# Kernel optimization log

Hardware: AMD Instinct MI355X
Metric: run time of the kernel (lower is better)

Reference implementation:

```python
import jax, jax.numpy as jnp
from jax import lax
import numpy as np

HID = 64      # hidden_size
IND = 25      # input_dim = 10 static + 15 dynamic features
HW = 25       # spatial size fixed by fc1 = Linear(12*12*hidden, ...)


def setup_inputs() -> dict:
    key = jax.random.key(0)
    ks = jax.random.split(key, 8)
    def rn(k, shape, s=0.05):
        return jax.random.normal(k, shape, dtype=jnp.float32) * s
    B, T = 64, 24
    return {
        "x": jax.random.normal(ks[0], (B, T, IND, HW, HW), dtype=jnp.float32),
        "ln_g": jnp.ones((IND,), jnp.float32),
        "ln_b": jnp.zeros((IND,), jnp.float32),
        "w_lstm1": rn(ks[1], (4 * HID, IND + HID, 3, 3)),
        "b_lstm1": jnp.zeros((4 * HID,), jnp.float32),
        "w_lstm2": rn(ks[2], (4 * HID, IND + HID, 3, 3)),
        "b_lstm2": jnp.zeros((4 * HID,), jnp.float32),
        "w_conv": rn(ks[3], (HID, 2 * HID, 3, 3)),
        "b_conv": jnp.zeros((HID,), jnp.float32),
        "w_fc1": rn(ks[4], (HID, 12 * 12 * HID)),
        "b_fc1": jnp.zeros((HID,), jnp.float32),
        "w_fc2": rn(ks[5], (HID // 2, HID)),
        "b_fc2": jnp.zeros((HID // 2,), jnp.float32),
        "w_fc3": rn(ks[6], (2, HID // 2)),
        "b_fc3": jnp.zeros((2,), jnp.float32),
    }


def _convlstm(x, w, b, dil):
    # x: (B, T, C, H, W); one ConvLSTM layer, zero-initialized states.
    # Gate order i, f, o, g (standard ndrplz ConvLSTM); same-padding 3x3 conv
    # with rhs dilation `dil` (padding = dil keeps HxW).
    B, _, _, H, W = x.shape
    h0 = jnp.zeros((B, HID, H, W), x.dtype)

    def step(carry, xt):
        h, c = carry
        z = lax.conv_general_dilated(
            jnp.concatenate([xt, h], axis=1), w, (1, 1),
            [(dil, dil), (dil, dil)], rhs_dilation=(dil, dil))
        z = z + b[None, :, None, None]
        i, f, o, g = jnp.split(z, 4, axis=1)
        c = jax.nn.sigmoid(f) * c + jax.nn.sigmoid(i) * jnp.tanh(g)
        h = jax.nn.sigmoid(o) * jnp.tanh(c)
        return (h, c), None

    (h, _), _ = lax.scan(step, (h0, h0), jnp.moveaxis(x, 1, 0))
    return h  # final hidden state (B, HID, H, W)


def reference(x, ln_g, ln_b, w_lstm1, b_lstm1, w_lstm2, b_lstm2,
              w_conv, b_conv, w_fc1, b_fc1, w_fc2, b_fc2, w_fc3, b_fc3):
    # LayerNorm over the channel dim (torch permutes C to last, LN, permutes back)
    mu = jnp.mean(x, axis=2, keepdims=True)
    var = jnp.var(x, axis=2, keepdims=True)
    xn = (x - mu) * lax.rsqrt(var + 1e-5)
    xn = xn * ln_g[None, None, :, None, None] + ln_b[None, None, :, None, None]

    h1 = _convlstm(xn, w_lstm1, b_lstm1, 1)   # dilation 1 branch
    h2 = _convlstm(xn, w_lstm2, b_lstm2, 2)   # dilation 2 branch
    h = jnp.concatenate([h1, h2], axis=1)     # (B, 2*HID, 25, 25)

    h = lax.conv_general_dilated(h, w_conv, (1, 1), [(1, 1), (1, 1)])
    h = jax.nn.relu(h + b_conv[None, :, None, None])
    # max_pool2d(2): floor(25/2)=12 -> VALID window 2 stride 2
    h = lax.reduce_window(h, -jnp.inf, lax.max, (1, 1, 2, 2), (1, 1, 2, 2), 'VALID')
    h = h.reshape(h.shape[0], -1)             # (B, 12*12*HID), channel-major like torch
    h = jax.nn.relu(h @ w_fc1.T + b_fc1)      # dropout is identity at inference
    h = jax.nn.relu(h @ w_fc2.T + b_fc2)
    h = h @ w_fc3.T + b_fc3
    return jax.nn.log_softmax(h, axis=1)
```

## Files before the change

kernel.cpp:

```cpp
#include <hip/hip_runtime.h>
#include <hip/hip_bf16.h>
#include <math.h>

#define B_    64
#define T_    24
#define IND_  25
#define HID_  64
#define NPIX  625

#define WP0   27
#define WP1   29
#define XSTR  32
#define HSTR  72
#define XROWS0 800
#define XROWS1 912
#define HROWS0 800
#define HROWS1 912
#define XB0   (XROWS0*XSTR)
#define XB1   (XROWS1*XSTR)
#define HB0   (HROWS0*HSTR)
#define HB1   (HROWS1*HSTR)
#define XB0T  (B_*XB0)
#define XB1T  (B_*XB1)
#define HB0T  (B_*HB0)
#define HB1T  (B_*HB1)
#define HPART (HB0T+HB1T)

#define NRG   9
#define RST0  144
#define RST1  212
#define CH0   (RST0*9)
#define CH1   (RST1*9)
#define XCH0  (RST0*4)
#define XCH1  (RST1*4)

#define HCROWS 832
#define HCB    (HCROWS*128)
#define HCTOT  (B_*HCB)

#define WFRAG_PER_BR (9*3*4*4*512)
#define WFRAG_TOT    (2*WFRAG_PER_BR)

typedef __bf16 bf16x8 __attribute__((ext_vector_type(8)));
typedef float  f32x4  __attribute__((ext_vector_type(4)));
typedef unsigned short ushort_t;
typedef unsigned int   uint_t;

typedef const __attribute__((address_space(1))) void as1_cvoid;
typedef __attribute__((address_space(3))) void as3_void;

__device__ __forceinline__ float sigmoidf_(float x) { return 1.f / (1.f + __expf(-x)); }
__device__ __forceinline__ float tanh_fast(float x) { return 2.f / (1.f + __expf(-2.f * x)) - 1.f; }
__device__ __forceinline__ ushort_t f2bf(float f) {
    unsigned int u = __float_as_uint(f);
    u += 0x7FFFu + ((u >> 16) & 1u);
    return (ushort_t)(u >> 16);
}

__global__ __launch_bounds__(256) void fill_zero_kernel(uint_t* __restrict__ p, int n) {
    int i = blockIdx.x * 256 + threadIdx.x;
    if (i < n) p[i] = 0u;
}

__global__ __launch_bounds__(256) void repack_w_kernel(
    const float* __restrict__ w1, const float* __restrict__ w2, ushort_t* __restrict__ Wfrag)
{
    int id = blockIdx.x * 256 + threadIdx.x;
    if (id >= WFRAG_TOT) return;
    int e    = id & 7;
    int lane = (id >> 3) & 63;
    int mf   = (id >> 9) & 3;
    int wm   = (id >> 11) & 3;
    int rest = id >> 13;
    int kk   = rest % 3;
    int tap  = (rest / 3) % 9;
    int br   = rest / 27;
    int l16 = lane & 15, kh = lane >> 4;
    int gate = mf;
    int oc   = wm * 16 + l16;
    int k    = kh * 8 + e;
    int c;
    if (kk == 0)      c = (k < IND_) ? k : -1;
    else if (kk == 1) c = IND_ + k;
    else              c = IND_ + 32 + k;
    const float* w = br ? w2 : w1;
    float v = (c >= 0) ? w[((size_t)(gate * 64 + oc) * 89 + c) * 9 + tap] : 0.f;
    Wfrag[id] = f2bf(v);
}

__global__ __launch_bounds__(256) void repack_wc_kernel(
    const float* __restrict__ wc, ushort_t* __restrict__ Wc)
{
    int id = blockIdx.x * 256 + threadIdx.x;
    if (id >= 9 * 64 * 128) return;
    int k   = id % 128;
    int oc  = (id / 128) % 64;
    int tap = id / (128 * 64);
    Wc[id] = f2bf(wc[((size_t)(oc * 128) + k) * 9 + tap]);
}

__global__ __launch_bounds__(256) void ln_t_kernel(
    const float* __restrict__ x, const float* __restrict__ gamma, const float* __restrict__ beta,
    ushort_t* __restrict__ xb0, ushort_t* __restrict__ xb1, int t)
{
    int p = blockIdx.x * 256 + threadIdx.x;
    if (p >= B_ * NPIX) return;
    int b = p / NPIX, hw = p % NPIX;
    int y = hw / 25, xx = hw % 25;
    const float* xp = x + ((size_t)(b * T_ + t) * IND_) * NPIX + hw;
    float v[IND_];
    float s = 0.f;
#pragma unroll
    for (int c = 0; c < IND_; ++c) { v[c] = xp[c * NPIX]; s += v[c]; }
    float mu = s * (1.f / IND_);
    float ss = 0.f;
#pragma unroll
    for (int c = 0; c < IND_; ++c) { float d = v[c] - mu; ss += d * d; }
    float rstd = rsqrtf(ss * (1.f / IND_) + 1e-5f);
    ushort_t* o0 = xb0 + (size_t)b * XB0 + (size_t)((y + 1) * WP0 + (xx + 1)) * XSTR;
    ushort_t* o1 = xb1 + (size_t)b * XB1 + (size_t)((y + 2) * WP1 + (xx + 2)) * XSTR;
#pragma unroll
    for (int c = 0; c < IND_; ++c) {
        ushort_t hv = f2bf((v[c] - mu) * rstd * gamma[c] + beta[c]);
        o0[c] = hv;
        o1[c] = hv;
    }
}

__global__ __launch_bounds__(512, 4) void convlstm_mfma_kernel(
    const float* __restrict__ x, const float* __restrict__ ln_g, const float* __restrict__ ln_b,
    ushort_t* __restrict__ xb0g, ushort_t* __restrict__ xb1g,
    const ushort_t* __restrict__ h0c, const ushort_t* __restrict__ h1c,
    ushort_t* __restrict__ h0n, ushort_t* __restrict__ h1n,
    const ushort_t* __restrict__ Wfrag,
    const float* __restrict__ bias1, const float* __restrict__ bias2,
    float* __restrict__ cst, int t)
{
    const int rg = blockIdx.x;
    const int b  = blockIdx.y;
    const int br = blockIdx.z;
    const int d  = 1 + br;
    const int Wp = 25 + 2 * d;
    const int par = t & 1, nxt = par ^ 1;
    const ushort_t* __restrict__ hc = (br ? h1c + (size_t)b * HB1 : h0c + (size_t)b * HB0);
    ushort_t* __restrict__ hn       = (br ? h1n + (size_t)b * HB1 : h0n + (size_t)b * HB0);
    const ushort_t* __restrict__ xbcur =
        br ? (xb1g + (size_t)par * XB1T + (size_t)b * XB1)
           : (xb0g + (size_t)par * XB0T + (size_t)b * XB0);
    const float* __restrict__ bias = br ? bias2 : bias1;
    const ushort_t* __restrict__ WFb = Wfrag + (size_t)br * WFRAG_PER_BR;
    f32x4* __restrict__ cb4 = (f32x4*)cst + (size_t)(br * B_ + b) * 16 * NPIX;

    __shared__ ushort_t tile[RST1 * HSTR];
    __shared__ ushort_t xtile[RST1 * XSTR];

    const int tid = threadIdx.x;
    const int u0  = rg * 3 * Wp;
    const int CH  = br ? CH1 : CH0;
    const int XCH = br ? XCH1 : XCH0;
    const int wave_u = tid & 448;

    {
        const char* gsrc = (const char*)(hc + (size_t)u0 * HSTR);
#pragma unroll
        for (int j = 0; j < 4; ++j) {
            const int i = j * 512 + tid;
            if (i < CH) {
                __builtin_amdgcn_global_load_lds(
                    (as1_cvoid*)(gsrc + (size_t)i * 16),
                    (as3_void*)((char*)tile + (size_t)(j * 512 + wave_u) * 16),
                    16, 0, 0);
            }
        }
    }
    {
        const char* gsrc = (const char*)(xbcur + (size_t)u0 * XSTR);
#pragma unroll
        for (int j = 0; j < 2; ++j) {
            const int i = j * 512 + tid;
            if (i < XCH) {
                __builtin_amdgcn_global_load_lds(
                    (as1_cvoid*)(gsrc + (size_t)i * 16),
                    (as3_void*)((char*)xtile + (size_t)(j * 512 + wave_u) * 16),
                    16, 0, 0);
            }
        }
    }
    if (t + 1 < T_ && tid < 35) {
        const int linbid = (br * B_ + b) * NRG + rg;
        const int p = linbid * 35 + tid;
        if (p < B_ * NPIX) {
            const int bb = p / NPIX, hw = p - bb * NPIX;
            const int y = hw / 25, xx = hw - y * 25;
            const float* xp = x + ((size_t)(bb * T_ + t + 1) * IND_) * NPIX + hw;
            float v[IND_];
            float s = 0.f;
#pragma unroll
            for (int c = 0; c < IND_; ++c) { v[c] = xp[c * NPIX]; s += v[c]; }
            const float mu = s * (1.f / IND_);
            float ss = 0.f;
#pragma unroll
            for (int c = 0; c < IND_; ++c) { float dd = v[c] - mu; ss += dd * dd; }
            const float rstd = rsqrtf(ss * (1.f / IND_) + 1e-5f);
            ushort_t us[IND_];
#pragma unroll
            for (int c = 0; c < IND_; ++c) us[c] = f2bf((v[c] - mu) * rstd * ln_g[c] + ln_b[c]);
            uint4 q0, q1, q2;
            q0.x = us[0] | ((uint_t)us[1] << 16);   q0.y = us[2] | ((uint_t)us[3] << 16);
            q0.z = us[4] | ((uint_t)us[5] << 16);   q0.w = us[6] | ((uint_t)us[7] << 16);
            q1.x = us[8] | ((uint_t)us[9] << 16);   q1.y = us[10] | ((uint_t)us[11] << 16);
            q1.z = us[12] | ((uint_t)us[13] << 16); q1.w = us[14] | ((uint_t)us[15] << 16);
            q2.x = us[16] | ((uint_t)us[17] << 16); q2.y = us[18] | ((uint_t)us[19] << 16);
            q2.z = us[20] | ((uint_t)us[21] << 16); q2.w = us[22] | ((uint_t)us[23] << 16);
            ushort_t* o0 = xb0g + (size_t)nxt * XB0T + (size_t)bb * XB0
                           + (size_t)((y + 1) * WP0 + (xx + 1)) * XSTR;
            ushort_t* o1 = xb1g + (size_t)nxt * XB1T + (size_t)bb * XB1
                           + (size_t)((y + 2) * WP1 + (xx + 2)) * XSTR;
            *(uint4*)o0 = q0; *(uint4*)(o0 + 8) = q1; *(uint4*)(o0 + 16) = q2; o0[24] = us[24];
            *(uint4*)o1 = q0; *(uint4*)(o1 + 8) = q1; *(uint4*)(o1 + 16) = q2; o1[24] = us[24];
        }
    }
    __syncthreads();

    const int w    = tid >> 6, lane = tid & 63;
    const int wm   = w & 3, wn = w >> 2;
    const int l16  = lane & 15, kh = lane >> 4;
    const int koff = kh * 8;

    f32x4 acc[4][3];
#pragma unroll
    for (int i = 0; i < 4; ++i)
#pragma unroll
        for (int j = 0; j < 3; ++j) acc[i][j] = (f32x4){0.f, 0.f, 0.f, 0.f};

    int baserel[3];
#pragma unroll
    for (int nf = 0; nf < 3; ++nf) {
        int n = wn * 48 + nf * 16 + l16;
        baserel[nf] = (n >> 5) * Wp + (n & 31);
    }

    const ushort_t* __restrict__ WTb = WFb + wm * 2048 + lane * 8;
    bf16x8 af[2][4];
#pragma unroll
    for (int mf = 0; mf < 4; ++mf)
        af[0][mf] = *(const bf16x8*)(WTb + mf * 512);

#pragma unroll
    for (int u = 0; u < 27; ++u) {
        if (u + 1 < 27) {
#pragma unroll
            for (int mf = 0; mf < 4; ++mf)
                af[(u + 1) & 1][mf] =
                    *(const bf16x8*)(WTb + (size_t)(u + 1) * 8192 + mf * 512);
        }
        const int tap = u / 3, kk = u - 3 * (u / 3);
        const int ky = tap / 3, kx = tap - 3 * ky;
        const int toff = (ky * Wp + kx) * d;
        bf16x8 bfr[3];
        if (kk == 0) {
#pragma unroll
            for (int nf = 0; nf < 3; ++nf)
                bfr[nf] = *(const bf16x8*)(xtile + (size_t)(baserel[nf] + toff) * XSTR + koff);
        } else {
#pragma unroll
            for (int nf = 0; nf < 3; ++nf)
                bfr[nf] = *(const bf16x8*)(tile + (baserel[nf] + toff) * HSTR
                                           + (kk - 1) * 32 + koff);
        }
#pragma unroll
        for (int mf = 0; mf < 4; ++mf)
#pragma unroll
            for (int nf = 0; nf < 3; ++nf)
                acc[mf][nf] = __builtin_amdgcn_mfma_f32_16x16x32_bf16(
                    af[u & 1][mf], bfr[nf], acc[mf][nf], 0, 0, 0);
    }

    const int oc0 = wm * 16 + kh * 4;
    const int ocq = wm * 4 + kh;
    float bi4[4], bf4[4], bo4[4], bg4[4];
#pragma unroll
    for (int r = 0; r < 4; ++r) {
        bi4[r] = bias[oc0 + r];
        bf4[r] = bias[64 + oc0 + r];
        bo4[r] = bias[128 + oc0 + r];
        bg4[r] = bias[192 + oc0 + r];
    }
#pragma unroll
    for (int nf = 0; nf < 3; ++nf) {
        const int n = wn * 48 + nf * 16 + l16;
        const int xx = n & 31;
        if (xx >= 25) continue;
        const int y = rg * 3 + (n >> 5);
        if (y >= 25) continue;
        const int pix = y * 25 + xx;
        f32x4* cp = cb4 + (size_t)ocq * NPIX + pix;
        f32x4 cv;
        if (t != 0) cv = *cp;
        else        cv = (f32x4){0.f, 0.f, 0.f, 0.f};
        ushort_t hs[4];
#pragma unroll
        for (int r = 0; r < 4; ++r) {
            const float zi = acc[0][nf][r] + bi4[r];
            const float zf = acc[1][nf][r] + bf4[r];
            const float zo = acc[2][nf][r] + bo4[r];
            const float zg = acc[3][nf][r] + bg4[r];
            const float cn = sigmoidf_(zf) * cv[r] + sigmoidf_(zi) * tanh_fast(zg);
            cv[r] = cn;
            hs[r] = f2bf(sigmoidf_(zo) * tanh_fast(cn));
        }
        *cp = cv;
        uint2 hv;
        hv.x = (uint_t)hs[0] | ((uint_t)hs[1] << 16);
        hv.y = (uint_t)hs[2] | ((uint_t)hs[3] << 16);
        *(uint2*)(hn + (size_t)((y + d) * Wp + (xx + d)) * HSTR + oc0) = hv;
    }
}

__global__ __launch_bounds__(256) void combine_h_kernel(
    const ushort_t* __restrict__ h0, const ushort_t* __restrict__ h1, ushort_t* __restrict__ Hc)
{
    int id = blockIdx.x * 256 + threadIdx.x;
    if (id >= B_ * NPIX * 128) return;
    int k   = id % 128;
    int pix = (id / 128) % NPIX;
    int b   = id / (128 * NPIX);
    int y = pix / 25, xx = pix % 25;
    ushort_t v;
    if (k < 64) v = h0[(size_t)b * HB0 + (size_t)((y + 1) * WP0 + (xx + 1)) * HSTR + k];
    else        v = h1[(size_t)b * HB1 + (size_t)((y + 2) * WP1 + (xx + 2)) * HSTR + (k - 64)];
    Hc[(size_t)b * HCB + (size_t)((y + 1) * 27 + (xx + 1)) * 128 + k] = v;
}

__global__ __launch_bounds__(512) void conv_mfma_kernel(
    const ushort_t* __restrict__ Hc, const ushort_t* __restrict__ Wc,
    const float* __restrict__ bc, float* __restrict__ conv_out)
{
    const int rg = blockIdx.x;
    const int b  = blockIdx.y;
    const ushort_t* __restrict__ Hb = Hc + (size_t)b * HCB;

    const int tid  = threadIdx.x;
    const int w    = tid >> 6, lane = tid & 63;
    const int wm   = w & 1, wn = w >> 1;
    const int l16  = lane & 15, kh = lane >> 4;
    const int koff = kh * 8;

    f32x4 acc[2][2];
#pragma unroll
    for (int i = 0; i < 2; ++i)
#pragma unroll
        for (int j = 0; j < 2; ++j) acc[i][j] = (f32x4){0.f, 0.f, 0.f, 0.f};

    int baserow[2];
#pragma unroll
    for (int nf = 0; nf < 2; ++nf) {
        int n = wn * 32 + nf * 16 + l16;
        baserow[nf] = (rg * 4 + (n >> 5)) * 27 + (n & 31);
    }
    const ushort_t* __restrict__ Wm = Wc + (size_t)(wm * 32 + l16) * 128 + koff;

    for (int tap = 0; tap < 9; ++tap) {
        const int ky = tap / 3, kx = tap - 3 * ky;
        const int toff = ky * 27 + kx;
        const ushort_t* __restrict__ Wt = Wm + (size_t)tap * (64 * 128);
        const ushort_t* Urow[2];
#pragma unroll
        for (int nf = 0; nf < 2; ++nf)
            Urow[nf] = Hb + (size_t)(baserow[nf] + toff) * 128 + koff;
#pragma unroll
        for (int kk = 0; kk < 4; ++kk) {
            bf16x8 af[2], bfr[2];
#pragma unroll
            for (int mf = 0; mf < 2; ++mf)
                af[mf] = *(const bf16x8*)(Wt + mf * 16 * 128 + kk * 32);
#pragma unroll
            for (int nf = 0; nf < 2; ++nf)
                bfr[nf] = *(const bf16x8*)(Urow[nf] + kk * 32);
#pragma unroll
            for (int mf = 0; mf < 2; ++mf)
#pragma unroll
                for (int nf = 0; nf < 2; ++nf)
                    acc[mf][nf] = __builtin_amdgcn_mfma_f32_16x16x32_bf16(
                        af[mf], bfr[nf], acc[mf][nf], 0, 0, 0);
        }
    }

#pragma unroll
    for (int mf = 0; mf < 2; ++mf) {
#pragma unroll
        for (int nf = 0; nf < 2; ++nf) {
            const int n = wn * 32 + nf * 16 + l16;
            const int xx = n & 31;
            if (xx >= 25) continue;
            const int y = rg * 4 + wn;
            if (y >= 25) continue;
#pragma unroll
            for (int r = 0; r < 4; ++r) {
                const int oc = wm * 32 + mf * 16 + kh * 4 + r;
                const float v = fmaxf(acc[mf][nf][r] + bc[oc], 0.f);
                conv_out[((size_t)(b * 64 + oc)) * NPIX + y * 25 + xx] = v;
            }
        }
    }
}

__global__ __launch_bounds__(256) void pool_kernel(
    const float* __restrict__ conv_out, float* __restrict__ pool)
{
    int id = blockIdx.x * 256 + threadIdx.x;
    if (id >= B_ * 64 * 144) return;
    int px = id % 12;
    int py = (id / 12) % 12;
    int oc = (id / 144) % 64;
    int b  = id / (144 * 64);
    const float* p = conv_out + ((size_t)(b * 64 + oc)) * NPIX;
    const int cy = 2 * py, cx = 2 * px;
    float mx = fmaxf(fmaxf(p[cy * 25 + cx], p[cy * 25 + cx + 1]),
                     fmaxf(p[(cy + 1) * 25 + cx], p[(cy + 1) * 25 + cx + 1]));
    pool[(size_t)b * 9216 + oc * 144 + py * 12 + px] = mx;
}

__global__ __launch_bounds__(256) void fc1_kernel(
    const float* __restrict__ pool, const float* __restrict__ w1, const float* __restrict__ b1,
    float* __restrict__ f1)
{
    const int task = blockIdx.x * 4 + (threadIdx.x >> 6);
    const int lane = threadIdx.x & 63;
    const int b = task >> 6, oc = task & 63;
    const float* pr = pool + (size_t)b * 9216;
    const float* wr = w1 + (size_t)oc * 9216;
    float acc = 0.f;
#pragma unroll 4
    for (int it = 0; it < 36; ++it) {
        const int k = it * 256 + lane * 4;
        const float4 p = *(const float4*)(pr + k);
        const float4 ww = *(const float4*)(wr + k);
        acc += p.x * ww.x + p.y * ww.y + p.z * ww.z + p.w * ww.w;
    }
#pragma unroll
    for (int off = 32; off > 0; off >>= 1) acc += __shfl_down(acc, off);
    if (lane == 0) f1[b * 64 + oc] = fmaxf(acc + b1[oc], 0.f);
}

__global__ __launch_bounds__(64) void head2_kernel(
    const float* __restrict__ f1,
    const float* __restrict__ w2, const float* __restrict__ b2,
    const float* __restrict__ w3, const float* __restrict__ b3,
    float* __restrict__ out)
{
    const int b = blockIdx.x;
    __shared__ float f1l[64];
    __shared__ float f2[32];
    const int tid = threadIdx.x;
    f1l[tid] = f1[b * 64 + tid];
    __syncthreads();
    if (tid < 32) {
        float acc = b2[tid];
        const float* wr = w2 + (size_t)tid * 64;
#pragma unroll
        for (int k = 0; k < 64; ++k) acc += f1l[k] * wr[k];
        f2[tid] = fmaxf(acc, 0.f);
    }
    __syncthreads();
    if (tid == 0) {
        float y0 = b3[0], y1 = b3[1];
#pragma unroll
        for (int k = 0; k < 32; ++k) { y0 += f2[k] * w3[k]; y1 += f2[k] * w3[32 + k]; }
        const float m = fmaxf(y0, y1);
        const float lse = m + logf(expf(y0 - m) + expf(y1 - m));
        out[b * 2 + 0] = y0 - lse;
        out[b * 2 + 1] = y1 - lse;
    }
}

extern "C" void kernel_launch(void* const* d_in, const int* in_sizes, int n_in,
                              void* d_out, int out_size, void* d_ws, size_t ws_size,
                              hipStream_t stream) {
    const float* x    = (const float*)d_in[0];
    const float* ln_g = (const float*)d_in[1];
    const float* ln_b = (const float*)d_in[2];
    const float* w_l1 = (const float*)d_in[3];
    const float* b_l1 = (const float*)d_in[4];
    const float* w_l2 = (const float*)d_in[5];
    const float* b_l2 = (const float*)d_in[6];
    const float* w_c  = (const float*)d_in[7];
    const float* b_c  = (const float*)d_in[8];
    const float* w_f1 = (const float*)d_in[9];
    const float* b_f1 = (const float*)d_in[10];
    const float* w_f2 = (const float*)d_in[11];
    const float* b_f2 = (const float*)d_in[12];
    const float* w_f3 = (const float*)d_in[13];
    const float* b_f3 = (const float*)d_in[14];

    ushort_t* wsu = (ushort_t*)d_ws;
    uint_t*   wsi = (uint_t*)d_ws;

    ushort_t* xb0 = wsu;
    ushort_t* xb1 = xb0 + 2 * (size_t)XB0T;
    ushort_t* h0A = xb1 + 2 * (size_t)XB1T;
    ushort_t* h1A = h0A + HB0T;
    ushort_t* h0B = h1A + HB1T;
    ushort_t* h1B = h0B + HB0T;
    float*    cst = (float*)(h1B + HB1T);
    float*    conv_out = cst;
    float*    pool = cst + 2560000;
    ushort_t* Wfrag = (ushort_t*)cst + 10240000;
    ushort_t* Wc    = Wfrag + WFRAG_TOT;
    float*    f1    = (float*)(Wc + 73728);
    ushort_t* Hc    = h0B;

    const size_t zt = 2 * (size_t)XB0T + 2 * (size_t)XB1T + 2 * (size_t)HPART;
    fill_zero_kernel<<<((int)(zt / 2) + 255) / 256, 256, 0, stream>>>(wsi, (int)(zt / 2));
    repack_w_kernel<<<(WFRAG_TOT + 255) / 256, 256, 0, stream>>>(w_l1, w_l2, Wfrag);
    repack_wc_kernel<<<(9 * 64 * 128 + 255) / 256, 256, 0, stream>>>(w_c, Wc);

    ln_t_kernel<<<(B_ * NPIX + 255) / 256, 256, 0, stream>>>(x, ln_g, ln_b, xb0, xb1, 0);

    ushort_t* H0[2] = {h0A, h0B};
    ushort_t* H1[2] = {h1A, h1B};
    for (int t = 0; t < T_; ++t) {
        const int cur = t & 1, nxt = cur ^ 1;
        convlstm_mfma_kernel<<<dim3(NRG, B_, 2), 512, 0, stream>>>(
            x, ln_g, ln_b, xb0, xb1,
            H0[cur], H1[cur], H0[nxt], H1[nxt], Wfrag, b_l1, b_l2, cst, t);
    }
    fill_zero_kernel<<<(HCTOT / 2 + 255) / 256, 256, 0, stream>>>((uint_t*)Hc, HCTOT / 2);
    combine_h_kernel<<<(B_ * NPIX * 128 + 255) / 256, 256, 0, stream>>>(h0A, h1A, Hc);
    conv_mfma_kernel<<<dim3(7, B_), 512, 0, stream>>>(Hc, Wc, b_c, conv_out);
    pool_kernel<<<(B_ * 64 * 144 + 255) / 256, 256, 0, stream>>>(conv_out, pool);
    fc1_kernel<<<1024, 256, 0, stream>>>(pool, w_f1, b_f1, f1);
    head2_kernel<<<B_, 64, 0, stream>>>(f1, w_f2, b_f2, w_f3, b_f3, (float*)d_out);
}
```

Before: 1.925 ms.

## Unify padded x buffer, read x directly from global, store cell state in fp16

Replaces the two per-branch padded bf16 input buffers with one buffer padded by 2, so each pixel's normalized input is written once. The convlstm kernel no longer stages the x tile in LDS and reads x fragments straight from global or L2 instead, which cuts LDS usage and the async load. The cell state is stored in fp16 rather than fp32, halving its read and write traffic each timestep. The trade-offs are uncoalesced global reads inside the MFMA loop and reduced precision in the recurrent cell state.

```diff
diff --git a/kernel.cpp b/kernel.cpp
--- a/kernel.cpp
+++ b/kernel.cpp
@@ -10,29 +10,25 @@
 
 #define WP0   27
 #define WP1   29
-#define XSTR  32
 #define HSTR  72
-#define XROWS0 800
-#define XROWS1 912
 #define HROWS0 800
 #define HROWS1 912
-#define XB0   (XROWS0*XSTR)
-#define XB1   (XROWS1*XSTR)
 #define HB0   (HROWS0*HSTR)
 #define HB1   (HROWS1*HSTR)
-#define XB0T  (B_*XB0)
-#define XB1T  (B_*XB1)
 #define HB0T  (B_*HB0)
 #define HB1T  (B_*HB1)
 #define HPART (HB0T+HB1T)
+
+#define WPX   29
+#define XROWSU 848
+#define XBU   (XROWSU*32)
+#define XBUT  (B_*XBU)
 
 #define NRG   9
 #define RST0  144
 #define RST1  212
 #define CH0   (RST0*9)
 #define CH1   (RST1*9)
-#define XCH0  (RST0*4)
-#define XCH1  (RST1*4)
 
 #define HCROWS 832
 #define HCB    (HCROWS*128)
@@ -43,6 +39,7 @@
 
 typedef __bf16 bf16x8 __attribute__((ext_vector_type(8)));
 typedef float  f32x4  __attribute__((ext_vector_type(4)));
+typedef _Float16 f16x4 __attribute__((ext_vector_type(4)));
 typedef unsigned short ushort_t;
 typedef unsigned int   uint_t;
 
@@ -101,7 +98,7 @@
 
 __global__ __launch_bounds__(256) void ln_t_kernel(
     const float* __restrict__ x, const float* __restrict__ gamma, const float* __restrict__ beta,
-    ushort_t* __restrict__ xb0, ushort_t* __restrict__ xb1, int t)
+    ushort_t* __restrict__ xbu, int t)
 {
     int p = blockIdx.x * 256 + threadIdx.x;
     if (p >= B_ * NPIX) return;
@@ -117,24 +114,20 @@
 #pragma unroll
     for (int c = 0; c < IND_; ++c) { float d = v[c] - mu; ss += d * d; }
     float rstd = rsqrtf(ss * (1.f / IND_) + 1e-5f);
-    ushort_t* o0 = xb0 + (size_t)b * XB0 + (size_t)((y + 1) * WP0 + (xx + 1)) * XSTR;
-    ushort_t* o1 = xb1 + (size_t)b * XB1 + (size_t)((y + 2) * WP1 + (xx + 2)) * XSTR;
-#pragma unroll
-    for (int c = 0; c < IND_; ++c) {
-        ushort_t hv = f2bf((v[c] - mu) * rstd * gamma[c] + beta[c]);
-        o0[c] = hv;
-        o1[c] = hv;
-    }
+    ushort_t* o = xbu + (size_t)b * XBU + (size_t)((y + 2) * WPX + (xx + 2)) * 32;
+#pragma unroll
+    for (int c = 0; c < IND_; ++c)
+        o[c] = f2bf((v[c] - mu) * rstd * gamma[c] + beta[c]);
 }
 
 __global__ __launch_bounds__(512, 4) void convlstm_mfma_kernel(
     const float* __restrict__ x, const float* __restrict__ ln_g, const float* __restrict__ ln_b,
-    ushort_t* __restrict__ xb0g, ushort_t* __restrict__ xb1g,
+    ushort_t* __restrict__ xbu,
     const ushort_t* __restrict__ h0c, const ushort_t* __restrict__ h1c,
     ushort_t* __restrict__ h0n, ushort_t* __restrict__ h1n,
     const ushort_t* __restrict__ Wfrag,
     const float* __restrict__ bias1, const float* __restrict__ bias2,
-    float* __restrict__ cst, int t)
+    ushort_t* __restrict__ cst, int t)
 {
     const int rg = blockIdx.x;
     const int b  = blockIdx.y;
@@ -144,20 +137,16 @@
     const int par = t & 1, nxt = par ^ 1;
     const ushort_t* __restrict__ hc = (br ? h1c + (size_t)b * HB1 : h0c + (size_t)b * HB0);
     ushort_t* __restrict__ hn       = (br ? h1n + (size_t)b * HB1 : h0n + (size_t)b * HB0);
-    const ushort_t* __restrict__ xbcur =
-        br ? (xb1g + (size_t)par * XB1T + (size_t)b * XB1)
-           : (xb0g + (size_t)par * XB0T + (size_t)b * XB0);
+    const ushort_t* __restrict__ xg = xbu + (size_t)par * XBUT + (size_t)b * XBU;
     const float* __restrict__ bias = br ? bias2 : bias1;
     const ushort_t* __restrict__ WFb = Wfrag + (size_t)br * WFRAG_PER_BR;
-    f32x4* __restrict__ cb4 = (f32x4*)cst + (size_t)(br * B_ + b) * 16 * NPIX;
+    f16x4* __restrict__ cb4 = (f16x4*)cst + (size_t)(br * B_ + b) * 16 * NPIX;
 
     __shared__ ushort_t tile[RST1 * HSTR];
-    __shared__ ushort_t xtile[RST1 * XSTR];
 
     const int tid = threadIdx.x;
     const int u0  = rg * 3 * Wp;
     const int CH  = br ? CH1 : CH0;
-    const int XCH = br ? XCH1 : XCH0;
     const int wave_u = tid & 448;
 
     {
@@ -169,19 +158,6 @@
                 __builtin_amdgcn_global_load_lds(
                     (as1_cvoid*)(gsrc + (size_t)i * 16),
                     (as3_void*)((char*)tile + (size_t)(j * 512 + wave_u) * 16),
-                    16, 0, 0);
-            }
-        }
-    }
-    {
-        const char* gsrc = (const char*)(xbcur + (size_t)u0 * XSTR);
-#pragma unroll
-        for (int j = 0; j < 2; ++j) {
-            const int i = j * 512 + tid;
-            if (i < XCH) {
-                __builtin_amdgcn_global_load_lds(
-                    (as1_cvoid*)(gsrc + (size_t)i * 16),
-                    (as3_void*)((char*)xtile + (size_t)(j * 512 + wave_u) * 16),
                     16, 0, 0);
             }
         }
@@ -212,12 +188,9 @@
             q1.z = us[12] | ((uint_t)us[13] << 16); q1.w = us[14] | ((uint_t)us[15] << 16);
             q2.x = us[16] | ((uint_t)us[17] << 16); q2.y = us[18] | ((uint_t)us[19] << 16);
             q2.z = us[20] | ((uint_t)us[21] << 16); q2.w = us[22] | ((uint_t)us[23] << 16);
-            ushort_t* o0 = xb0g + (size_t)nxt * XB0T + (size_t)bb * XB0
-                           + (size_t)((y + 1) * WP0 + (xx + 1)) * XSTR;
-            ushort_t* o1 = xb1g + (size_t)nxt * XB1T + (size_t)bb * XB1
-                           + (size_t)((y + 2) * WP1 + (xx + 2)) * XSTR;
-            *(uint4*)o0 = q0; *(uint4*)(o0 + 8) = q1; *(uint4*)(o0 + 16) = q2; o0[24] = us[24];
-            *(uint4*)o1 = q0; *(uint4*)(o1 + 8) = q1; *(uint4*)(o1 + 16) = q2; o1[24] = us[24];
+            ushort_t* o = xbu + (size_t)nxt * XBUT + (size_t)bb * XBU
+                          + (size_t)((y + 2) * WPX + (xx + 2)) * 32;
+            *(uint4*)o = q0; *(uint4*)(o + 8) = q1; *(uint4*)(o + 16) = q2; o[24] = us[24];
         }
     }
     __syncthreads();
@@ -234,10 +207,13 @@
         for (int j = 0; j < 3; ++j) acc[i][j] = (f32x4){0.f, 0.f, 0.f, 0.f};
 
     int baserel[3];
+    int basex[3];
 #pragma unroll
     for (int nf = 0; nf < 3; ++nf) {
         int n = wn * 48 + nf * 16 + l16;
-        baserel[nf] = (n >> 5) * Wp + (n & 31);
+        const int rit = n >> 5, xxa = n & 31;
+        baserel[nf] = rit * Wp + xxa;
+        basex[nf] = ((rg * 3 + rit + 2) * WPX + (xxa + 2)) * 32 + koff;
     }
 
     const ushort_t* __restrict__ WTb = WFb + wm * 2048 + lane * 8;
@@ -256,13 +232,14 @@
         }
         const int tap = u / 3, kk = u - 3 * (u / 3);
         const int ky = tap / 3, kx = tap - 3 * ky;
-        const int toff = (ky * Wp + kx) * d;
         bf16x8 bfr[3];
         if (kk == 0) {
+            const int toffx = ((ky - 1) * WPX + (kx - 1)) * d * 32;
 #pragma unroll
             for (int nf = 0; nf < 3; ++nf)
-                bfr[nf] = *(const bf16x8*)(xtile + (size_t)(baserel[nf] + toff) * XSTR + koff);
+                bfr[nf] = *(const bf16x8*)(xg + (size_t)(basex[nf] + toffx));
         } else {
+            const int toff = (ky * Wp + kx) * d;
 #pragma unroll
             for (int nf = 0; nf < 3; ++nf)
                 bfr[nf] = *(const bf16x8*)(tile + (baserel[nf] + toff) * HSTR
@@ -294,10 +271,10 @@
         const int y = rg * 3 + (n >> 5);
         if (y >= 25) continue;
         const int pix = y * 25 + xx;
-        f32x4* cp = cb4 + (size_t)ocq * NPIX + pix;
-        f32x4 cv;
-        if (t != 0) cv = *cp;
-        else        cv = (f32x4){0.f, 0.f, 0.f, 0.f};
+        f16x4* cp = cb4 + (size_t)ocq * NPIX + pix;
+        f16x4 cvh;
+        if (t != 0) cvh = *cp;
+        else        cvh = (f16x4){0, 0, 0, 0};
         ushort_t hs[4];
 #pragma unroll
         for (int r = 0; r < 4; ++r) {
@@ -305,11 +282,11 @@
             const float zf = acc[1][nf][r] + bf4[r];
             const float zo = acc[2][nf][r] + bo4[r];
             const float zg = acc[3][nf][r] + bg4[r];
-            const float cn = sigmoidf_(zf) * cv[r] + sigmoidf_(zi) * tanh_fast(zg);
-            cv[r] = cn;
+            const float cn = sigmoidf_(zf) * (float)cvh[r] + sigmoidf_(zi) * tanh_fast(zg);
+            cvh[r] = (_Float16)cn;
             hs[r] = f2bf(sigmoidf_(zo) * tanh_fast(cn));
         }
-        *cp = cv;
+        *cp = cvh;
         uint2 hv;
         hv.x = (uint_t)hs[0] | ((uint_t)hs[1] << 16);
         hv.y = (uint_t)hs[2] | ((uint_t)hs[3] << 16);
@@ -496,33 +473,32 @@
     ushort_t* wsu = (ushort_t*)d_ws;
     uint_t*   wsi = (uint_t*)d_ws;
 
-    ushort_t* xb0 = wsu;
-    ushort_t* xb1 = xb0 + 2 * (size_t)XB0T;
-    ushort_t* h0A = xb1 + 2 * (size_t)XB1T;
+    ushort_t* xbu = wsu;
+    ushort_t* h0A = xbu + 2 * (size_t)XBUT;
     ushort_t* h1A = h0A + HB0T;
     ushort_t* h0B = h1A + HB1T;
     ushort_t* h1B = h0B + HB0T;
-    float*    cst = (float*)(h1B + HB1T);
-    float*    conv_out = cst;
-    float*    pool = cst + 2560000;
-    ushort_t* Wfrag = (ushort_t*)cst + 10240000;
+    ushort_t* cst = h1B + HB1T;
+    ushort_t* Wfrag = cst + 5120000;
     ushort_t* Wc    = Wfrag + WFRAG_TOT;
     float*    f1    = (float*)(Wc + 73728);
     ushort_t* Hc    = h0B;
-
-    const size_t zt = 2 * (size_t)XB0T + 2 * (size_t)XB1T + 2 * (size_t)HPART;
+    float*    conv_out = (float*)cst;
+    float*    pool  = (float*)wsu;
+
+    const size_t zt = 2 * (size_t)XBUT + 2 * (size_t)HPART;
     fill_zero_kernel<<<((int)(zt / 2) + 255) / 256, 256, 0, stream>>>(wsi, (int)(zt / 2));
     repack_w_kernel<<<(WFRAG_TOT + 255) / 256, 256, 0, stream>>>(w_l1, w_l2, Wfrag);
     repack_wc_kernel<<<(9 * 64 * 128 + 255) / 256, 256, 0, stream>>>(w_c, Wc);
 
-    ln_t_kernel<<<(B_ * NPIX + 255) / 256, 256, 0, stream>>>(x, ln_g, ln_b, xb0, xb1, 0);
+    ln_t_kernel<<<(B_ * NPIX + 255) / 256, 256, 0, stream>>>(x, ln_g, ln_b, xbu, 0);
 
     ushort_t* H0[2] = {h0A, h0B};
     ushort_t* H1[2] = {h1A, h1B};
     for (int t = 0; t < T_; ++t) {
         const int cur = t & 1, nxt = cur ^ 1;
         convlstm_mfma_kernel<<<dim3(NRG, B_, 2), 512, 0, stream>>>(
-            x, ln_g, ln_b, xb0, xb1,
+            x, ln_g, ln_b, xbu,
             H0[cur], H1[cur], H0[nxt], H1[nxt], Wfrag, b_l1, b_l2, cst, t);
     }
     fill_zero_kernel<<<(HCTOT / 2 + 255) / 256, 256, 0, stream>>>((uint_t*)Hc, HCTOT / 2);
```

Measured after the change: 2.087 ms. +8.4%, slower.
